# Performance work log

Measured on AMD Instinct MI355X. Metric: run time of the kernel, lower is better.

Reference implementation:

```python
import jax, jax.numpy as jnp
import numpy as np

B, S, D, H, DH, CACHE = 2, 2048, 1024, 16, 64, 2048
MAX_KV = 4096
F16_MAX = 65504.0  # tf.float16.max, used as the additive mask penalty in the original


def setup_inputs() -> dict:
    key = jax.random.key(0)
    ks = jax.random.split(key, 9)
    s = 0.02
    return {
        "q": jax.random.normal(ks[0], (B, S, D), jnp.float32),
        "k": jax.random.normal(ks[1], (B, S, D), jnp.float32),
        "v": jax.random.normal(ks[2], (B, S, D), jnp.float32),
        "cache_k": jax.random.normal(ks[3], (B, 1, CACHE, DH), jnp.float32),
        "cache_v": jax.random.normal(ks[4], (B, 1, CACHE, DH), jnp.float32),
        "wq": jax.random.normal(ks[5], (D, H * DH), jnp.float32) * s,
        "wk": jax.random.normal(ks[6], (D, DH), jnp.float32) * s,
        "wv": jax.random.normal(ks[7], (D, DH), jnp.float32) * s,
        "wo": jax.random.normal(ks[8], (H * DH, D), jnp.float32) * s,
    }


def reference(q, k, v, cache_k, cache_v, wq, wk, wv, wo):
    scale = 1.0 / np.sqrt(DH).astype(np.float32)
    b, s = q.shape[0], q.shape[1]
    # projections
    qh = (q @ wq).reshape(b, s, H, DH).transpose(0, 2, 1, 3)        # [B,H,S,dh]
    kh = (k @ wk).reshape(b, s, 1, DH).transpose(0, 2, 1, 3)        # [B,1,S,dh]
    vh = (v @ wv).reshape(b, s, 1, DH).transpose(0, 2, 1, 3)        # [B,1,S,dh]
    # KV cache concat + truncate to max_kv_length
    kc = jnp.concatenate([cache_k, kh], axis=2)[:, :, -MAX_KV:, :]  # [B,1,K,dh]
    vc = jnp.concatenate([cache_v, vh], axis=2)[:, :, -MAX_KV:, :]
    kk = kc[:, 0]  # [B,K,dh]  (single shared KV head)
    vv = vc[:, 0]
    # scores: [B,H,S,K]
    scores = jnp.einsum("bhqd,bkd->bhqk", qh, kk) * scale
    # causal mask exactly as tf.linalg.band_part(ones, -1, 0): mask[i,j] = j <= i
    klen = kk.shape[1]
    causal = jnp.tril(jnp.ones((s, klen), bool))                    # [S,K]
    scores = scores - (1.0 - causal.astype(scores.dtype)) * F16_MAX
    att = jax.nn.softmax(scores, axis=-1)
    vals = jnp.einsum("bhqk,bkd->bhqd", att, vv)                    # [B,H,S,dh]
    vals = vals.transpose(0, 2, 1, 3).reshape(b, s, H * DH)
    out = vals @ wo                                                 # [B,S,D]
    return out, kc, vc
```

## Files before the change

kernel.cpp:

```cpp
#include <hip/hip_runtime.h>
#include <hip/hip_bf16.h>
#include <type_traits>

#define B_ 2
#define S_ 2048
#define D_ 1024
#define H_ 16
#define DH_ 64
#define CACHE_ 2048
#define MAXKV_ 4096

using f32x4  = __attribute__((ext_vector_type(4))) float;
using bf16x8 = __attribute__((ext_vector_type(8))) short;
using bf16x4 = __attribute__((ext_vector_type(4))) short;

__device__ inline short f2bf(float x) {
  __hip_bfloat16 h = __float2bfloat16(x);
  short r;
  __builtin_memcpy(&r, &h, 2);
  return r;
}
__device__ inline void stor(float* p, float x) { *p = x; }
__device__ inline void stor(__hip_bfloat16* p, float x) { *p = __float2bfloat16(x); }

__device__ inline void glds16(const short* g, short* l) {
  __builtin_amdgcn_global_load_lds(
      (const __attribute__((address_space(1))) void*)g,
      (__attribute__((address_space(3))) void*)l, 16, 0, 0);
}

__device__ inline void tile_transpose(const float* __restrict__ in,
                                      short* __restrict__ out, int R, int C,
                                      int r0, int c0, int t, float T[64][65]) {
#pragma unroll
  for (int p = 0; p < 16; ++p) {
    int li = t + p * 256;
    int r = li >> 6, c = li & 63;
    T[r][c] = in[(size_t)(r0 + r) * C + c0 + c];
  }
  __syncthreads();
#pragma unroll
  for (int p = 0; p < 16; ++p) {
    int li = t + p * 256;
    int c = li >> 6, r = li & 63;
    out[(size_t)(c0 + c) * R + r0 + r] = f2bf(T[r][c]);
  }
}

__global__ __launch_bounds__(256) void prep_kernel(
    const float* __restrict__ q, const float* __restrict__ ck,
    const float* __restrict__ cv, const float* __restrict__ wq,
    const float* __restrict__ wk, const float* __restrict__ wv,
    const float* __restrict__ wo, short* __restrict__ qbf,
    float4* __restrict__ kc, float4* __restrict__ vc,
    short* __restrict__ ckbf, short* __restrict__ cvT,
    short* __restrict__ wqT, short* __restrict__ wkT,
    short* __restrict__ wvT, short* __restrict__ woT) {
  __shared__ float T[64][65];
  const int bx = blockIdx.x, t = threadIdx.x;
  if (bx < 1024) {
    int base = bx * 4096 + t * 4;
#pragma unroll
    for (int p = 0; p < 4; ++p) {
      int i = base + p * 1024;
      float4 f = *(const float4*)&q[i];
      bf16x4 s;
      s[0] = f2bf(f.x); s[1] = f2bf(f.y); s[2] = f2bf(f.z); s[3] = f2bf(f.w);
      *(bf16x4*)&qbf[i] = s;
    }
  } else if (bx < 1280) {
    int idx = (bx - 1024) * 256 + t;
    const int per_b = CACHE_ * DH_ / 4;
    int b = idx / per_b, rem = idx % per_b;
    int dst = b * (MAXKV_ * DH_ / 4) + rem;
    float4 a = ((const float4*)ck)[idx], c = ((const float4*)cv)[idx];
    kc[dst] = a;
    vc[dst] = c;
    bf16x4 s;
    s[0] = f2bf(a.x); s[1] = f2bf(a.y); s[2] = f2bf(a.z); s[3] = f2bf(a.w);
    *(bf16x4*)&ckbf[idx * 4] = s;
  } else if (bx < 1344) {
    int tt = bx - 1280;
    int b = tt >> 5, tile = tt & 31;
    tile_transpose(cv + (size_t)b * CACHE_ * DH_, cvT + (size_t)b * DH_ * CACHE_,
                   CACHE_, DH_, tile * 64, 0, t, T);
  } else if (bx < 1856) {
    int tt = bx - 1344;
    int sel = tt >> 8;
    tt &= 255;
    tile_transpose(sel ? wo : wq, sel ? woT : wqT, D_, D_, (tt >> 4) * 64,
                   (tt & 15) * 64, t, T);
  } else {
    int tt = bx - 1856;
    int sel = tt >> 4, tile = tt & 15;
    tile_transpose(sel ? wv : wk, sel ? wvT : wkT, D_, DH_, tile * 64, 0, t, T);
  }
}

__global__ __launch_bounds__(256) void gemm_kv(
    const float* __restrict__ A, const short* __restrict__ Bt,
    float* __restrict__ C, int K, const float* __restrict__ A2,
    const short* __restrict__ Bt2, float* __restrict__ C2) {
  if (blockIdx.z) { A = A2; Bt = Bt2; C = C2; }
  __shared__ __align__(16) short As[32 * 72];
  __shared__ __align__(16) short Bs[64 * 72];
  const int t = threadIdx.x;
  const int w = t >> 6, lane = t & 63, lx = lane & 15, quad = lane >> 4;
  const int row_base = (w & 1) * 16, col_base = (w >> 1) * 32;
  const int row0 = blockIdx.x * 32;

  f32x4 acc[2];
  acc[0] = (f32x4){0.f, 0.f, 0.f, 0.f};
  acc[1] = (f32x4){0.f, 0.f, 0.f, 0.f};

  for (int k0 = 0; k0 < K; k0 += 64) {
    {
      int row = t >> 3, c0 = (t & 7) * 8;
      const float* src = &A[(size_t)(row0 + row) * K + k0 + c0];
      float4 f0 = *(const float4*)src;
      float4 f1 = *(const float4*)(src + 4);
      bf16x4 s0, s1;
      s0[0] = f2bf(f0.x); s0[1] = f2bf(f0.y); s0[2] = f2bf(f0.z); s0[3] = f2bf(f0.w);
      s1[0] = f2bf(f1.x); s1[1] = f2bf(f1.y); s1[2] = f2bf(f1.z); s1[3] = f2bf(f1.w);
      *(bf16x4*)&As[row * 72 + c0] = s0;
      *(bf16x4*)&As[row * 72 + c0 + 4] = s1;
    }
    {
      int row = t >> 2, c0 = (t & 3) * 16;
      const short* src = &Bt[(size_t)row * K + k0 + c0];
      *(bf16x8*)&Bs[row * 72 + c0] = *(const bf16x8*)src;
      *(bf16x8*)&Bs[row * 72 + c0 + 8] = *(const bf16x8*)(src + 8);
    }
    __syncthreads();
#pragma unroll
    for (int kb = 0; kb < 2; ++kb) {
      bf16x8 a = *(bf16x8*)&As[(row_base + lx) * 72 + kb * 32 + quad * 8];
#pragma unroll
      for (int cb = 0; cb < 2; ++cb) {
        bf16x8 b = *(bf16x8*)&Bs[(col_base + cb * 16 + lx) * 72 + kb * 32 + quad * 8];
        acc[cb] = __builtin_amdgcn_mfma_f32_16x16x32_bf16(a, b, acc[cb], 0, 0, 0);
      }
    }
    __syncthreads();
  }

#pragma unroll
  for (int cb = 0; cb < 2; ++cb)
#pragma unroll
    for (int reg = 0; reg < 4; ++reg) {
      int r = row0 + row_base + quad * 4 + reg;
      int c = col_base + cb * 16 + lx;
      int bb = r >> 11, s = r & 2047;
      C[(size_t)bb * (MAXKV_ * DH_) + (size_t)(CACHE_ + s) * DH_ + c] =
          acc[cb][reg];
    }
}

template <typename TC>
__global__ __launch_bounds__(256) void gemm_glds(
    const short* __restrict__ A, const short* __restrict__ Bt,
    TC* __restrict__ C, int M, int N, int K, float scale) {
  __shared__ __align__(16) short As[2][128 * 32];
  __shared__ __align__(16) short Bs[2][64 * 32];
  const int t = threadIdx.x;
  const int w = t >> 6, lane = t & 63, lx = lane & 15, quad = lane >> 4;
  const int row0 = blockIdx.x * 128, col0 = blockIdx.y * 64;
  const int row_base = (w >> 1) * 64, col_base = (w & 1) * 32;

  const short* Ag = A + (size_t)(row0 + w * 32 + (lane >> 2)) * K + (lane & 3) * 8;
  const short* Bg = Bt + (size_t)(col0 + w * 16 + (lane >> 2)) * K + (lane & 3) * 8;
  short* Al0 = &As[0][(w * 32) * 32];
  short* Al1 = &As[1][(w * 32) * 32];
  short* Bl0 = &Bs[0][(w * 16) * 32];
  short* Bl1 = &Bs[1][(w * 16) * 32];

  f32x4 acc[4][2];
#pragma unroll
  for (int mb = 0; mb < 4; ++mb)
#pragma unroll
    for (int cb = 0; cb < 2; ++cb) acc[mb][cb] = (f32x4){0.f, 0.f, 0.f, 0.f};

  for (int k0 = 0; k0 < K; k0 += 64) {
    glds16(Ag + k0, Al0);
    glds16(Ag + 16 * K + k0, Al0 + 16 * 32);
    glds16(Ag + k0 + 32, Al1);
    glds16(Ag + 16 * K + k0 + 32, Al1 + 16 * 32);
    glds16(Bg + k0, Bl0);
    glds16(Bg + k0 + 32, Bl1);
    __syncthreads();
    bf16x8 a[4][2], b[2][2];
#pragma unroll
    for (int mb = 0; mb < 4; ++mb)
#pragma unroll
      for (int kb = 0; kb < 2; ++kb)
        a[mb][kb] = *(bf16x8*)&As[kb][(row_base + mb * 16 + lx) * 32 + quad * 8];
#pragma unroll
    for (int cb = 0; cb < 2; ++cb)
#pragma unroll
      for (int kb = 0; kb < 2; ++kb)
        b[cb][kb] = *(bf16x8*)&Bs[kb][(col_base + cb * 16 + lx) * 32 + quad * 8];
#pragma unroll
    for (int kb = 0; kb < 2; ++kb)
#pragma unroll
      for (int mb = 0; mb < 4; ++mb)
#pragma unroll
        for (int cb = 0; cb < 2; ++cb)
          acc[mb][cb] = __builtin_amdgcn_mfma_f32_16x16x32_bf16(
              a[mb][kb], b[cb][kb], acc[mb][cb], 0, 0, 0);
    __syncthreads();
  }

#pragma unroll
  for (int mb = 0; mb < 4; ++mb)
#pragma unroll
    for (int cb = 0; cb < 2; ++cb)
#pragma unroll
      for (int reg = 0; reg < 4; ++reg) {
        int r = row0 + row_base + mb * 16 + quad * 4 + reg;
        int c = col0 + col_base + cb * 16 + lx;
        stor(&C[(size_t)r * N + c], acc[mb][cb][reg] * scale);
      }
}

__global__ __launch_bounds__(256) void attention_mfma(
    __hip_bfloat16* __restrict__ qh,
    const short* __restrict__ ckbf,
    const short* __restrict__ cvT) {
  __shared__ __align__(16) short Ks[64 * 72];
  __shared__ __align__(16) short Vt[64 * 72];
  __shared__ __align__(16) short Ps[64 * 72];
  const int t = threadIdx.x;
  const int w = t >> 6, lane = t & 63, lx = lane & 15, quad = lane >> 4;
  const int p = blockIdx.x, bh = blockIdx.y;
  const int b = bh >> 4, h = bh & 15;
  const int qtA = p, qtB = 31 - p;
  const int q0A = qtA * 64, q0B = qtB * 64;
  short* qhp = (short*)qh;

  bf16x8 aqA[2], aqB[2];
#pragma unroll
  for (int kb = 0; kb < 2; ++kb) {
    aqA[kb] = *(const bf16x8*)&qhp[(size_t)(b * S_ + q0A + w * 16 + lx) * (H_ * DH_) +
                                   h * DH_ + kb * 32 + quad * 8];
    aqB[kb] = *(const bf16x8*)&qhp[(size_t)(b * S_ + q0B + w * 16 + lx) * (H_ * DH_) +
                                   h * DH_ + kb * 32 + quad * 8];
  }

  f32x4 oA[4], oB[4];
#pragma unroll
  for (int d = 0; d < 4; ++d) {
    oA[d] = (f32x4){0.f, 0.f, 0.f, 0.f};
    oB[d] = (f32x4){0.f, 0.f, 0.f, 0.f};
  }
  float lA[4] = {0.f, 0.f, 0.f, 0.f}, lB[4] = {0.f, 0.f, 0.f, 0.f};

  for (int kt = 0; kt <= qtB; ++kt) {
    const int k0 = kt * 64;
#pragma unroll
    for (int pp = 0; pp < 2; ++pp) {
      int li = t + pp * 256;
      int row = li >> 3, kk0 = (li & 7) * 8;
      *(bf16x8*)&Ks[row * 72 + kk0] =
          *(const bf16x8*)&ckbf[(size_t)(b * CACHE_ + k0 + row) * DH_ + kk0];
      *(bf16x8*)&Vt[row * 72 + kk0] =
          *(const bf16x8*)&cvT[(size_t)(b * DH_ + row) * CACHE_ + k0 + kk0];
    }
    __syncthreads();

    bf16x8 bk[4][2], bv[4][2];
#pragma unroll
    for (int cb = 0; cb < 4; ++cb)
#pragma unroll
      for (int kb = 0; kb < 2; ++kb) {
        bk[cb][kb] = *(bf16x8*)&Ks[(cb * 16 + lx) * 72 + kb * 32 + quad * 8];
        bv[cb][kb] = *(bf16x8*)&Vt[(cb * 16 + lx) * 72 + kb * 32 + quad * 8];
      }

    {
      f32x4 accs[4];
#pragma unroll
      for (int cb = 0; cb < 4; ++cb) accs[cb] = (f32x4){0.f, 0.f, 0.f, 0.f};
#pragma unroll
      for (int cb = 0; cb < 4; ++cb)
#pragma unroll
        for (int kb = 0; kb < 2; ++kb)
          accs[cb] = __builtin_amdgcn_mfma_f32_16x16x32_bf16(aqB[kb], bk[cb][kb],
                                                             accs[cb], 0, 0, 0);
      const bool diag = (kt == qtB);
#pragma unroll
      for (int cb = 0; cb < 4; ++cb)
#pragma unroll
        for (int reg = 0; reg < 4; ++reg) {
          float x = accs[cb][reg];
          if (diag && (cb * 16 + lx > w * 16 + quad * 4 + reg)) x = -1e30f;
          float pe = __expf(x - 10.0f);
          Ps[(w * 16 + quad * 4 + reg) * 72 + cb * 16 + lx] = f2bf(pe);
          lB[reg] += pe;
        }
#pragma unroll
      for (int kb = 0; kb < 2; ++kb) {
        bf16x8 ap = *(bf16x8*)&Ps[(w * 16 + lx) * 72 + kb * 32 + quad * 8];
#pragma unroll
        for (int d = 0; d < 4; ++d)
          oB[d] = __builtin_amdgcn_mfma_f32_16x16x32_bf16(ap, bv[d][kb], oB[d], 0, 0, 0);
      }
    }

    if (kt <= qtA) {
      f32x4 accs[4];
#pragma unroll
      for (int cb = 0; cb < 4; ++cb) accs[cb] = (f32x4){0.f, 0.f, 0.f, 0.f};
#pragma unroll
      for (int cb = 0; cb < 4; ++cb)
#pragma unroll
        for (int kb = 0; kb < 2; ++kb)
          accs[cb] = __builtin_amdgcn_mfma_f32_16x16x32_bf16(aqA[kb], bk[cb][kb],
                                                             accs[cb], 0, 0, 0);
      const bool diag = (kt == qtA);
#pragma unroll
      for (int cb = 0; cb < 4; ++cb)
#pragma unroll
        for (int reg = 0; reg < 4; ++reg) {
          float x = accs[cb][reg];
          if (diag && (cb * 16 + lx > w * 16 + quad * 4 + reg)) x = -1e30f;
          float pe = __expf(x - 10.0f);
          Ps[(w * 16 + quad * 4 + reg) * 72 + cb * 16 + lx] = f2bf(pe);
          lA[reg] += pe;
        }
#pragma unroll
      for (int kb = 0; kb < 2; ++kb) {
        bf16x8 ap = *(bf16x8*)&Ps[(w * 16 + lx) * 72 + kb * 32 + quad * 8];
#pragma unroll
        for (int d = 0; d < 4; ++d)
          oA[d] = __builtin_amdgcn_mfma_f32_16x16x32_bf16(ap, bv[d][kb], oA[d], 0, 0, 0);
      }
    }
    __syncthreads();
  }

#pragma unroll
  for (int off = 1; off < 16; off <<= 1)
#pragma unroll
    for (int reg = 0; reg < 4; ++reg) {
      lA[reg] += __shfl_xor(lA[reg], off, 64);
      lB[reg] += __shfl_xor(lB[reg], off, 64);
    }

#pragma unroll
  for (int d = 0; d < 4; ++d)
#pragma unroll
    for (int reg = 0; reg < 4; ++reg) {
      int col = h * DH_ + d * 16 + lx;
      int qA = q0A + w * 16 + quad * 4 + reg;
      int qB = q0B + w * 16 + quad * 4 + reg;
      qhp[(size_t)(b * S_ + qA) * (H_ * DH_) + col] = f2bf(oA[d][reg] / lA[reg]);
      qhp[(size_t)(b * S_ + qB) * (H_ * DH_) + col] = f2bf(oB[d][reg] / lB[reg]);
    }
}

extern "C" void kernel_launch(void* const* d_in, const int* in_sizes, int n_in,
                              void* d_out, int out_size, void* d_ws, size_t ws_size,
                              hipStream_t stream) {
  const float* q  = (const float*)d_in[0];
  const float* k  = (const float*)d_in[1];
  const float* v  = (const float*)d_in[2];
  const float* ck = (const float*)d_in[3];
  const float* cv = (const float*)d_in[4];
  const float* wq = (const float*)d_in[5];
  const float* wk = (const float*)d_in[6];
  const float* wv = (const float*)d_in[7];
  const float* wo = (const float*)d_in[8];

  float* out = (float*)d_out;
  float* kc  = out + (size_t)B_ * S_ * D_;
  float* vc  = kc + (size_t)B_ * MAXKV_ * DH_;

  short* qbf = (short*)d_out;

  short* ws   = (short*)d_ws;
  short* qh   = ws;
  short* ckbf = qh + (size_t)B_ * S_ * H_ * DH_;
  short* cvT  = ckbf + (size_t)B_ * CACHE_ * DH_;
  short* wqT  = cvT + (size_t)B_ * CACHE_ * DH_;
  short* wkT  = wqT + (size_t)D_ * H_ * DH_;
  short* wvT  = wkT + (size_t)D_ * DH_;
  short* woT  = wvT + (size_t)D_ * DH_;

  prep_kernel<<<1888, 256, 0, stream>>>(q, ck, cv, wq, wk, wv, wo, qbf,
                                        (float4*)kc, (float4*)vc, ckbf, cvT,
                                        wqT, wkT, wvT, woT);
  gemm_kv<<<dim3(128, 1, 2), 256, 0, stream>>>(k, wkT, kc, D_, v, wvT, vc);
  gemm_glds<__hip_bfloat16><<<dim3(32, 16), 256, 0, stream>>>(
      qbf, wqT, (__hip_bfloat16*)qh, B_ * S_, H_ * DH_, D_, 0.125f);
  attention_mfma<<<dim3(16, B_ * H_), 256, 0, stream>>>(
      (__hip_bfloat16*)qh, ckbf, cvT);
  gemm_glds<float><<<dim3(32, 16), 256, 0, stream>>>(
      qh, woT, out, B_ * S_, D_, D_, 1.0f);
}
```

Measured before the change: 208.7 us.

## Interleave A/B score MFMAs with separate P buffers, swizzle P, use exp2

Splits the shared P buffer into separate A and B tiles so both query tiles' QK^T MFMAs can be issued back to back before the softmax and PV stages, which gives more independent MFMA work to overlap with exponentials and LDS traffic. P writes and reads use an XOR swizzle to reduce LDS bank conflicts. The exponential switches to exp2 with log2(e) folded into the Q projection scale. The cost is an extra 9 KB of LDS and more live accumulator registers, which may reduce occupancy.

```diff
diff --git a/kernel.cpp b/kernel.cpp
--- a/kernel.cpp
+++ b/kernel.cpp
@@ -228,7 +228,8 @@
     const short* __restrict__ cvT) {
   __shared__ __align__(16) short Ks[64 * 72];
   __shared__ __align__(16) short Vt[64 * 72];
-  __shared__ __align__(16) short Ps[64 * 72];
+  __shared__ __align__(16) short PsA[64 * 72];
+  __shared__ __align__(16) short PsB[64 * 72];
   const int t = threadIdx.x;
   const int w = t >> 6, lane = t & 63, lx = lane & 15, quad = lane >> 4;
   const int p = blockIdx.x, bh = blockIdx.y;
@@ -237,6 +238,9 @@
   const int q0A = qtA * 64, q0B = qtB * 64;
   short* qhp = (short*)qh;
 
+  const int wsz = (quad >> 1) & 1;
+  const int rsz = ((lx >> 3) & 1) << 4;
+
   bf16x8 aqA[2], aqB[2];
 #pragma unroll
   for (int kb = 0; kb < 2; ++kb) {
@@ -276,60 +280,66 @@
         bv[cb][kb] = *(bf16x8*)&Vt[(cb * 16 + lx) * 72 + kb * 32 + quad * 8];
       }
 
+    const bool actA = (kt <= qtA);
+
+    f32x4 accsB[4], accsA[4];
+#pragma unroll
+    for (int cb = 0; cb < 4; ++cb) accsB[cb] = (f32x4){0.f, 0.f, 0.f, 0.f};
+#pragma unroll
+    for (int cb = 0; cb < 4; ++cb)
+#pragma unroll
+      for (int kb = 0; kb < 2; ++kb)
+        accsB[cb] = __builtin_amdgcn_mfma_f32_16x16x32_bf16(aqB[kb], bk[cb][kb],
+                                                            accsB[cb], 0, 0, 0);
+    if (actA) {
+#pragma unroll
+      for (int cb = 0; cb < 4; ++cb) accsA[cb] = (f32x4){0.f, 0.f, 0.f, 0.f};
+#pragma unroll
+      for (int cb = 0; cb < 4; ++cb)
+#pragma unroll
+        for (int kb = 0; kb < 2; ++kb)
+          accsA[cb] = __builtin_amdgcn_mfma_f32_16x16x32_bf16(aqA[kb], bk[cb][kb],
+                                                              accsA[cb], 0, 0, 0);
+    }
+
     {
-      f32x4 accs[4];
-#pragma unroll
-      for (int cb = 0; cb < 4; ++cb) accs[cb] = (f32x4){0.f, 0.f, 0.f, 0.f};
+      const bool diag = (kt == qtB);
 #pragma unroll
       for (int cb = 0; cb < 4; ++cb)
 #pragma unroll
-        for (int kb = 0; kb < 2; ++kb)
-          accs[cb] = __builtin_amdgcn_mfma_f32_16x16x32_bf16(aqB[kb], bk[cb][kb],
-                                                             accs[cb], 0, 0, 0);
-      const bool diag = (kt == qtB);
-#pragma unroll
-      for (int cb = 0; cb < 4; ++cb)
-#pragma unroll
         for (int reg = 0; reg < 4; ++reg) {
-          float x = accs[cb][reg];
+          float x = accsB[cb][reg];
           if (diag && (cb * 16 + lx > w * 16 + quad * 4 + reg)) x = -1e30f;
-          float pe = __expf(x - 10.0f);
-          Ps[(w * 16 + quad * 4 + reg) * 72 + cb * 16 + lx] = f2bf(pe);
+          float pe = exp2f(x - 14.4269504089f);
+          PsB[(w * 16 + quad * 4 + reg) * 72 + (cb ^ wsz) * 16 + lx] = f2bf(pe);
           lB[reg] += pe;
         }
-#pragma unroll
-      for (int kb = 0; kb < 2; ++kb) {
-        bf16x8 ap = *(bf16x8*)&Ps[(w * 16 + lx) * 72 + kb * 32 + quad * 8];
-#pragma unroll
-        for (int d = 0; d < 4; ++d)
-          oB[d] = __builtin_amdgcn_mfma_f32_16x16x32_bf16(ap, bv[d][kb], oB[d], 0, 0, 0);
-      }
-    }
-
-    if (kt <= qtA) {
-      f32x4 accs[4];
-#pragma unroll
-      for (int cb = 0; cb < 4; ++cb) accs[cb] = (f32x4){0.f, 0.f, 0.f, 0.f};
+    }
+    if (actA) {
+      const bool diag = (kt == qtA);
 #pragma unroll
       for (int cb = 0; cb < 4; ++cb)
 #pragma unroll
-        for (int kb = 0; kb < 2; ++kb)
-          accs[cb] = __builtin_amdgcn_mfma_f32_16x16x32_bf16(aqA[kb], bk[cb][kb],
-                                                             accs[cb], 0, 0, 0);
-      const bool diag = (kt == qtA);
-#pragma unroll
-      for (int cb = 0; cb < 4; ++cb)
-#pragma unroll
         for (int reg = 0; reg < 4; ++reg) {
-          float x = accs[cb][reg];
+          float x = accsA[cb][reg];
           if (diag && (cb * 16 + lx > w * 16 + quad * 4 + reg)) x = -1e30f;
-          float pe = __expf(x - 10.0f);
-          Ps[(w * 16 + quad * 4 + reg) * 72 + cb * 16 + lx] = f2bf(pe);
+          float pe = exp2f(x - 14.4269504089f);
+          PsA[(w * 16 + quad * 4 + reg) * 72 + (cb ^ wsz) * 16 + lx] = f2bf(pe);
           lA[reg] += pe;
         }
+    }
+
+#pragma unroll
+    for (int kb = 0; kb < 2; ++kb) {
+      bf16x8 ap = *(bf16x8*)&PsB[(w * 16 + lx) * 72 + ((kb * 32 + quad * 8) ^ rsz)];
+#pragma unroll
+      for (int d = 0; d < 4; ++d)
+        oB[d] = __builtin_amdgcn_mfma_f32_16x16x32_bf16(ap, bv[d][kb], oB[d], 0, 0, 0);
+    }
+    if (actA) {
 #pragma unroll
       for (int kb = 0; kb < 2; ++kb) {
-        bf16x8 ap = *(bf16x8*)&Ps[(w * 16 + lx) * 72 + kb * 32 + quad * 8];
+        bf16x8 ap = *(bf16x8*)&PsA[(w * 16 + lx) * 72 + ((kb * 32 + quad * 8) ^ rsz)];
 #pragma unroll
         for (int d = 0; d < 4; ++d)
           oA[d] = __builtin_amdgcn_mfma_f32_16x16x32_bf16(ap, bv[d][kb], oA[d], 0, 0, 0);
@@ -391,7 +401,7 @@
                                         wqT, wkT, wvT, woT);
   gemm_kv<<<dim3(128, 1, 2), 256, 0, stream>>>(k, wkT, kc, D_, v, wvT, vc);
   gemm_glds<__hip_bfloat16><<<dim3(32, 16), 256, 0, stream>>>(
-      qbf, wqT, (__hip_bfloat16*)qh, B_ * S_, H_ * DH_, D_, 0.125f);
+      qbf, wqT, (__hip_bfloat16*)qh, B_ * S_, H_ * DH_, D_, 0.18033688f);
   attention_mfma<<<dim3(16, B_ * H_), 256, 0, stream>>>(
       (__hip_bfloat16*)qh, ckbf, cvT);
   gemm_glds<float><<<dim3(32, 16), 256, 0, stream>>>(
```

Measured after the change: 214.8 us. +2.9%, slower.
